# Performance work log

Hardware: AMD Instinct MI355X
Metric: run time of the kernel (lower is better)

Reference implementation:

```python
import jax, jax.numpy as jnp
import numpy as np

DIM, HEADS, SEQ_LEN = 768, 12, 4096
HEAD_DIM = DIM // HEADS
RMS_EPS = 1.1920928955078125e-07  # torch fp32 finfo eps (default for F.rms_norm)
ATTN_SCALE = 0.12


def _rms_norm(x):
    # F.rms_norm(x, (x.size(-1),)) with no weight
    return x * jax.lax.rsqrt(jnp.mean(x * x, axis=-1, keepdims=True) + RMS_EPS)


def _rotary_tables(T, head_dim):
    # angular_freq: (1/1024)**linspace(0,1,head_dim//4) padded with zeros to head_dim//2
    freqs = (1.0 / 1024.0) ** jnp.linspace(0.0, 1.0, head_dim // 4, dtype=jnp.float32)
    freqs = jnp.concatenate([freqs, jnp.zeros(head_dim // 4, dtype=jnp.float32)])
    t = jnp.arange(T, dtype=jnp.float32)
    theta = t[:, None] * freqs[None, :]  # [T, head_dim//2]
    return jnp.cos(theta), jnp.sin(theta)


def _apply_rotary(x, cos, sin):
    # x: [B, T, H, D]; cos/sin: [T, D//2]
    x1, x2 = jnp.split(x.astype(jnp.float32), 2, axis=-1)
    c = cos[None, :, None, :]
    s = sin[None, :, None, :]
    y1 = x1 * c + x2 * s
    y2 = -x1 * s + x2 * c
    return jnp.concatenate([y1, y2], axis=-1).astype(x.dtype)


def setup_inputs() -> dict:
    key = jax.random.key(0)
    k1, k2, k3 = jax.random.split(key, 3)
    x = jax.random.normal(k1, (1, SEQ_LEN, DIM), dtype=jnp.float32)
    std = 0.5 * DIM ** (-0.5)
    bound = (3.0 ** 0.5) * std
    qkv_w = jax.random.uniform(k2, (3, DIM, DIM), dtype=jnp.float32, minval=-bound, maxval=bound)
    # c_proj is zero-initialized in the module; use small random weights for a nontrivial baseline
    c_proj_w = jax.random.normal(k3, (DIM, DIM), dtype=jnp.float32) * (DIM ** -0.5)
    return {"x": x, "qkv_w": qkv_w, "c_proj_w": c_proj_w}


def reference(x, qkv_w, c_proj_w):
    B, T, dim = x.shape
    H, D = HEADS, HEAD_DIM
    # fused QKV: F.linear(x, qkv_w.flatten(end_dim=1)) -> x @ W^T, split into q,k,v
    qkv = jnp.einsum('btd,kfd->btkf', x, qkv_w)  # [B, T, 3, dim]
    qkv = qkv.reshape(B, T, 3, H, D)
    q, k, v = qkv[:, :, 0], qkv[:, :, 1], qkv[:, :, 2]  # each [B, T, H, D]
    q, k = _rms_norm(q), _rms_norm(k)
    cos, sin = _rotary_tables(T, D)
    q, k = _apply_rotary(q, cos, sin), _apply_rotary(k, cos, sin)
    # causal attention with scale=0.12 (flex_attention with causal block mask)
    scores = jnp.einsum('bthd,bshd->bhts', q, k) * ATTN_SCALE  # [B, H, T, T]
    causal = jnp.tril(jnp.ones((T, T), dtype=bool))
    scores = jnp.where(causal[None, None], scores, jnp.finfo(scores.dtype).min)
    probs = jax.nn.softmax(scores, axis=-1)
    y = jnp.einsum('bhts,bshd->bthd', probs, v).reshape(B, T, dim)
    return y @ c_proj_w.T
```

## Files before the change

kernel.cpp:

```cpp
#include <hip/hip_runtime.h>
#include <math.h>


typedef __bf16 bf16;
typedef __bf16 bf16x4 __attribute__((ext_vector_type(4)));
typedef __bf16 bf16x8 __attribute__((ext_vector_type(8)));
typedef float  f32x4  __attribute__((ext_vector_type(4)));

#define MFMA_BF16(a, b, c) __builtin_amdgcn_mfma_f32_16x16x32_bf16((a), (b), (c), 0, 0, 0)

#define SEQ  4096
#define NH   12
#define HD   64
#define DM   768
#define NQKV 2304
#define NPART 4
#define ATTN_SCALE 0.12f
#define LOG2E 1.4426950408889634f
#define RMS_EPS 1.1920928955078125e-07f

typedef __attribute__((address_space(3))) void  lds_void;
typedef const __attribute__((address_space(1))) void g_void;

__device__ __forceinline__ void gload16(const void* g, void* l)
{
  __builtin_amdgcn_global_load_lds((g_void*)g, (lds_void*)l, 16, 0, 0);
}

__global__ __launch_bounds__(256) void convert_in(const float* __restrict__ src,
                                                  bf16* __restrict__ dst, int n)
{
  const int i0 = (blockIdx.x * 256 + threadIdx.x) * 8;
  if (i0 >= n) return;
  f32x4 a = *(const f32x4*)(src + i0);
  f32x4 b = *(const f32x4*)(src + i0 + 4);
  bf16x8 o;
#pragma unroll
  for (int j = 0; j < 4; j++) { o[j] = (bf16)a[j]; o[j + 4] = (bf16)b[j]; }
  *(bf16x8*)(dst + i0) = o;
}

__device__ __forceinline__ void gemm128_core(
    const bf16* __restrict__ A, const bf16* __restrict__ B,
    int m0, int n0, bf16 (*As)[32], bf16 (*Bs)[32], f32x4 acc[4][4])
{
  const int tid = threadIdx.x;
  const int lane = tid & 63, w = tid >> 6;
  const int c16 = lane & 15, q4 = lane >> 4;
  const int mo = (w & 1) * 64, no = (w >> 1) * 64;
  const int srow = tid >> 2, scol = (tid & 3) * 8;
  const f32x4 vzero = {0.f, 0.f, 0.f, 0.f};
#pragma unroll
  for (int i = 0; i < 4; i++)
#pragma unroll
    for (int j = 0; j < 4; j++) acc[i][j] = vzero;

  const bf16* aBase = A + (size_t)(m0 + srow) * DM + scol;
  const bf16* bBase = B + (size_t)(n0 + srow) * DM + scol;

  for (int k0 = 0; k0 < DM; k0 += 32) {
    gload16(aBase + k0,                 &As[srow][scol]);
    gload16(aBase + (size_t)64 * DM + k0, &As[srow + 64][scol]);
    gload16(bBase + k0,                 &Bs[srow][scol]);
    gload16(bBase + (size_t)64 * DM + k0, &Bs[srow + 64][scol]);
    __syncthreads();
    bf16x8 ar[4], br[4];
#pragma unroll
    for (int mq = 0; mq < 4; mq++)
      ar[mq] = *(const bf16x8*)&As[mo + mq * 16 + c16][q4 * 8];
#pragma unroll
    for (int nq = 0; nq < 4; nq++)
      br[nq] = *(const bf16x8*)&Bs[no + nq * 16 + c16][q4 * 8];
#pragma unroll
    for (int mq = 0; mq < 4; mq++)
#pragma unroll
      for (int nq = 0; nq < 4; nq++)
        acc[mq][nq] = MFMA_BF16(ar[mq], br[nq], acc[mq][nq]);
    __syncthreads();
  }
}

__global__ __launch_bounds__(256) void gemm_qkv(
    const bf16* __restrict__ A, const bf16* __restrict__ B,
    bf16* __restrict__ Qb, bf16* __restrict__ Kb, bf16* __restrict__ Vt)
{
  __shared__ bf16 As[128][32];
  __shared__ bf16 Bs[128][32];
  const int m0 = blockIdx.x * 128, n0 = blockIdx.y * 128;
  f32x4 acc[4][4];
  gemm128_core(A, B, m0, n0, As, Bs, acc);

  const int lane = threadIdx.x & 63, w = threadIdx.x >> 6;
  const int c16 = lane & 15, q4 = lane >> 4;
  const int mo = (w & 1) * 64, no = (w >> 1) * 64;
  const int kidx = blockIdx.y / 6;
  const int rr0 = (n0 - kidx * DM) + no;
  const int h = rr0 >> 6;

  if (kidx == 2) {
#pragma unroll
    for (int nq = 0; nq < 4; nq++) {
      const int d = nq * 16 + c16;
#pragma unroll
      for (int mq = 0; mq < 4; mq++) {
        const int mb = m0 + mo + mq * 16 + q4 * 4;
#pragma unroll
        for (int rg = 0; rg < 4; rg++)
          Vt[((h * HD) + d) * SEQ + mb + rg] = (bf16)acc[mq][nq][rg];
      }
    }
  } else {
    bf16* dst = kidx ? Kb : Qb;
    const float scale = kidx ? 1.0f : (ATTN_SCALE * LOG2E);
    const float fr = exp2f(-10.0f * (float)c16 * (1.0f / 15.0f));
#pragma unroll
    for (int mq = 0; mq < 4; mq++) {
#pragma unroll
      for (int rg = 0; rg < 4; rg++) {
        const int m = m0 + mo + mq * 16 + q4 * 4 + rg;
        const float x0 = acc[mq][0][rg], x1 = acc[mq][1][rg];
        const float x2 = acc[mq][2][rg], x3 = acc[mq][3][rg];
        float ss = x0 * x0 + x1 * x1 + x2 * x2 + x3 * x3;
        ss += __shfl_xor(ss, 1, 64);
        ss += __shfl_xor(ss, 2, 64);
        ss += __shfl_xor(ss, 4, 64);
        ss += __shfl_xor(ss, 8, 64);
        const float rinv = rsqrtf(ss * (1.0f / 64.0f) + RMS_EPS) * scale;
        const float xn0 = x0 * rinv, xn1 = x1 * rinv;
        const float xn2 = x2 * rinv, xn3 = x3 * rinv;
        float sn, cs;
        sincosf((float)m * fr, &sn, &cs);
        const float y0 = xn0 * cs + xn2 * sn;
        const float y2 = xn2 * cs - xn0 * sn;
        bf16* rp = dst + (size_t)(h * SEQ + m) * HD + c16;
        rp[0]  = (bf16)y0;
        rp[16] = (bf16)xn1;
        rp[32] = (bf16)y2;
        rp[48] = (bf16)xn3;
      }
    }
  }
}

__global__ __launch_bounds__(256) void gemm_proj(
    const bf16* __restrict__ A, const bf16* __restrict__ B, float* __restrict__ C)
{
  __shared__ bf16 As[128][32];
  __shared__ bf16 Bs[128][32];
  const int m0 = blockIdx.x * 128, n0 = blockIdx.y * 128;
  f32x4 acc[4][4];
  gemm128_core(A, B, m0, n0, As, Bs, acc);

  const int lane = threadIdx.x & 63, w = threadIdx.x >> 6;
  const int c16 = lane & 15, q4 = lane >> 4;
  const int mo = (w & 1) * 64, no = (w >> 1) * 64;
#pragma unroll
  for (int nq = 0; nq < 4; nq++) {
    const int n = n0 + no + nq * 16 + c16;
#pragma unroll
    for (int mq = 0; mq < 4; mq++) {
      const int mb = m0 + mo + mq * 16 + q4 * 4;
#pragma unroll
      for (int rg = 0; rg < 4; rg++)
        C[(size_t)(mb + rg) * DM + n] = acc[mq][nq][rg];
    }
  }
}

__global__ __launch_bounds__(256, 3) void flash_partial(
    const bf16* __restrict__ Qb, const bf16* __restrict__ Kb,
    const bf16* __restrict__ Vt, bf16* __restrict__ Opart,
    float* __restrict__ Lpart)
{
  __shared__ bf16 Ks[64][72];
  __shared__ bf16 Vts[64][72];
  __shared__ bf16 Pst[4][32][68];
  const int h = blockIdx.y, p = blockIdx.z;
  const int jb = blockIdx.x;
  const int tid = threadIdx.x;
  const int lane = tid & 63, w = tid >> 6;
  const int c16 = lane & 15, q4 = lane >> 4;
  const int sr = tid >> 3, sc8 = (tid & 7) * 8;

  const bf16* Kbase = Kb + (size_t)h * SEQ * HD;
  const bf16* Vbase = Vt + (size_t)h * HD * SEQ;
  const f32x4 vzero = {0.f, 0.f, 0.f, 0.f};

#pragma unroll 1
  for (int half = 0; half < 2; ++half) {
    const int qi = half ? jb : (31 - jb);
    const int q0 = qi * 128;

    bf16x8 aq[2][2];
#pragma unroll
    for (int f = 0; f < 2; f++) {
      const int tq = q0 + w * 32 + f * 16 + c16;
      aq[f][0] = *(const bf16x8*)&Qb[((h * SEQ) + tq) * HD + q4 * 8];
      aq[f][1] = *(const bf16x8*)&Qb[((h * SEQ) + tq) * HD + 32 + q4 * 8];
    }
    const int qg[2] = { q0 + w * 32 + c16, q0 + w * 32 + 16 + c16 };
    const int qb[2] = { q0 + w * 32,       q0 + w * 32 + 16 };

    f32x4 O[2][4];
    float l_f[2] = {0.f, 0.f};
#pragma unroll
    for (int f = 0; f < 2; f++)
#pragma unroll
      for (int j = 0; j < 4; j++) O[f][j] = vzero;

    const int sEnd = q0 + 64;
    const int sBeg = p * 64;
    if (sBeg <= sEnd) {
      bf16x8 kr0 = *(const bf16x8*)&Kbase[(sBeg + sr) * HD + sc8];
      bf16x8 kr1 = *(const bf16x8*)&Kbase[(sBeg + sr + 32) * HD + sc8];
      bf16x8 vr0 = *(const bf16x8*)&Vbase[sr * SEQ + sBeg + sc8];
      bf16x8 vr1 = *(const bf16x8*)&Vbase[(sr + 32) * SEQ + sBeg + sc8];

      for (int s0 = sBeg; s0 <= sEnd; s0 += NPART * 64) {
        __syncthreads();
        *(bf16x8*)&Ks[sr][sc8]       = kr0;
        *(bf16x8*)&Ks[sr + 32][sc8]  = kr1;
        *(bf16x8*)&Vts[sr][sc8]      = vr0;
        *(bf16x8*)&Vts[sr + 32][sc8] = vr1;
        __syncthreads();

        const int snext = s0 + NPART * 64;
        if (snext <= sEnd) {
          kr0 = *(const bf16x8*)&Kbase[(snext + sr) * HD + sc8];
          kr1 = *(const bf16x8*)&Kbase[(snext + sr + 32) * HD + sc8];
          vr0 = *(const bf16x8*)&Vbase[sr * SEQ + snext + sc8];
          vr1 = *(const bf16x8*)&Vbase[(sr + 32) * SEQ + snext + sc8];
        }

        bf16x8 kf0[4], kf1[4];
#pragma unroll
        for (int nt = 0; nt < 4; nt++) {
          kf0[nt] = *(const bf16x8*)&Ks[nt * 16 + c16][q4 * 8];
          kf1[nt] = *(const bf16x8*)&Ks[nt * 16 + c16][32 + q4 * 8];
        }
#pragma unroll
        for (int f = 0; f < 2; f++) {
          f32x4 S[4];
          __builtin_amdgcn_s_setprio(1);
#pragma unroll
          for (int nt = 0; nt < 4; nt++) {
            f32x4 z = vzero;
            z = MFMA_BF16(kf0[nt], aq[f][0], z);
            z = MFMA_BF16(kf1[nt], aq[f][1], z);
            S[nt] = z;
          }
          __builtin_amdgcn_s_setprio(0);
          float lf = l_f[f];
          if (s0 + 63 <= qb[f]) {
#pragma unroll
            for (int nt = 0; nt < 4; nt++) {
#pragma unroll
              for (int rg = 0; rg < 4; rg++) {
                const float pv = exp2f(S[nt][rg]);
                S[nt][rg] = pv;
                lf += pv;
              }
              bf16x4 pk = { (bf16)S[nt][0], (bf16)S[nt][1], (bf16)S[nt][2], (bf16)S[nt][3] };
              *(bf16x4*)&Pst[w][f * 16 + c16][nt * 16 + q4 * 4] = pk;
            }
          } else if (s0 > qb[f] + 15) {
            const bf16x4 zk = { (bf16)0.f, (bf16)0.f, (bf16)0.f, (bf16)0.f };
#pragma unroll
            for (int nt = 0; nt < 4; nt++)
              *(bf16x4*)&Pst[w][f * 16 + c16][nt * 16 + q4 * 4] = zk;
          } else {
#pragma unroll
            for (int nt = 0; nt < 4; nt++) {
#pragma unroll
              for (int rg = 0; rg < 4; rg++) {
                const int s_g = s0 + nt * 16 + q4 * 4 + rg;
                const float pv = (s_g > qg[f]) ? 0.f : exp2f(S[nt][rg]);
                S[nt][rg] = pv;
                lf += pv;
              }
              bf16x4 pk = { (bf16)S[nt][0], (bf16)S[nt][1], (bf16)S[nt][2], (bf16)S[nt][3] };
              *(bf16x4*)&Pst[w][f * 16 + c16][nt * 16 + q4 * 4] = pk;
            }
          }
          l_f[f] = lf;
        }
        bf16x8 ap[2][2];
#pragma unroll
        for (int f = 0; f < 2; f++) {
          ap[f][0] = *(const bf16x8*)&Pst[w][f * 16 + c16][q4 * 8];
          ap[f][1] = *(const bf16x8*)&Pst[w][f * 16 + c16][32 + q4 * 8];
        }
#pragma unroll
        for (int dt = 0; dt < 4; dt++) {
          bf16x8 bv0 = *(const bf16x8*)&Vts[dt * 16 + c16][q4 * 8];
          bf16x8 bv1 = *(const bf16x8*)&Vts[dt * 16 + c16][32 + q4 * 8];
          __builtin_amdgcn_s_setprio(1);
#pragma unroll
          for (int f = 0; f < 2; f++) {
            O[f][dt] = MFMA_BF16(ap[f][0], bv0, O[f][dt]);
            O[f][dt] = MFMA_BF16(ap[f][1], bv1, O[f][dt]);
          }
          __builtin_amdgcn_s_setprio(0);
        }
      }
    }

#pragma unroll
    for (int f = 0; f < 2; f++) {
      float l = l_f[f];
      l += __shfl_xor(l, 16, 64);
      l += __shfl_xor(l, 32, 64);
      l_f[f] = l;
    }
    const int u = ((h * 32 + qi) * NPART + p);
    bf16* Op = Opart + (size_t)u * 8192;
#pragma unroll
    for (int f = 0; f < 2; f++)
#pragma unroll
      for (int dt = 0; dt < 4; dt++)
#pragma unroll
        for (int rg = 0; rg < 4; rg++)
          Op[(w * 32 + f * 16 + q4 * 4 + rg) * 64 + dt * 16 + c16] = (bf16)O[f][dt][rg];
    if (lane < 32) {
      if (q4 == 0) {
#pragma unroll
        for (int f = 0; f < 2; f++)
          Lpart[u * 128 + w * 32 + f * 16 + c16] = l_f[f];
      }
    }
  }
}

__global__ __launch_bounds__(256) void flash_combine(
    const bf16* __restrict__ Opart, const float* __restrict__ Lpart,
    bf16* __restrict__ Y)
{
  const int q64 = blockIdx.x, h = blockIdx.y;
  const int qi = q64 >> 1, roff = (q64 & 1) * 64;
  const int row = threadIdx.x >> 2, cg = (threadIdx.x & 3) * 16;
  const int u0 = (h * 32 + qi) * NPART;
  const int r128 = roff + row;
  float lsum = 0.f;
#pragma unroll
  for (int p = 0; p < NPART; p++) lsum += Lpart[(u0 + p) * 128 + r128];
  const float inv = 1.0f / lsum;
  const bf16* O0 = Opart + (size_t)u0 * 8192 + r128 * 64 + cg;
  bf16* yp = Y + (size_t)(q64 * 64 + row) * DM + h * HD + cg;
#pragma unroll
  for (int j = 0; j < 16; j += 8) {
    float s[8] = {0, 0, 0, 0, 0, 0, 0, 0};
#pragma unroll
    for (int p = 0; p < NPART; p++) {
      bf16x8 a = *(const bf16x8*)(O0 + p * 8192 + j);
#pragma unroll
      for (int e = 0; e < 8; e++) s[e] += (float)a[e];
    }
#pragma unroll
    for (int e = 0; e < 8; e++) yp[j + e] = (bf16)(s[e] * inv);
  }
}

extern "C" void kernel_launch(void* const* d_in, const int* in_sizes, int n_in,
                              void* d_out, int out_size, void* d_ws, size_t ws_size,
                              hipStream_t stream)
{
  (void)in_sizes; (void)n_in; (void)out_size; (void)ws_size;
  const float* x      = (const float*)d_in[0];
  const float* qkvw   = (const float*)d_in[1];
  const float* cprojw = (const float*)d_in[2];
  float* outp = (float*)d_out;

  const int NX = SEQ * DM, NW = NQKV * DM, NP = DM * DM;

  char* ws = (char*)d_ws;
  bf16*  xb    = (bf16*)(ws);
  bf16*  wqkv  = (bf16*)(ws + 6291456);
  bf16*  wproj = (bf16*)(ws + 9830400);
  bf16*  Q     = (bf16*)(ws + 11010048);
  bf16*  K     = (bf16*)(ws + 17301504);
  bf16*  Vt    = (bf16*)(ws + 23592960);
  bf16*  Y     = (bf16*)(ws + 29884416);
  bf16*  Opart = (bf16*)(ws + 36175872);
  float* Lpart = (float*)(ws + 61341696);

  convert_in<<<dim3(NX / 2048), 256, 0, stream>>>(x,      xb,    NX);
  convert_in<<<dim3(NW / 2048), 256, 0, stream>>>(qkvw,   wqkv,  NW);
  convert_in<<<dim3(NP / 2048), 256, 0, stream>>>(cprojw, wproj, NP);

  gemm_qkv     <<<dim3(SEQ / 128, NQKV / 128), 256, 0, stream>>>(xb, wqkv, Q, K, Vt);
  flash_partial<<<dim3(16, NH, NPART),         256, 0, stream>>>(Q, K, Vt, Opart, Lpart);
  flash_combine<<<dim3(SEQ / 64, NH),          256, 0, stream>>>(Opart, Lpart, Y);
  gemm_proj    <<<dim3(SEQ / 128, DM / 128),   256, 0, stream>>>(Y, wproj, outp);
}
```

Measured before the change: 180.5 us.

## Fuse input conversions, swizzle block order, retile projection GEMM, raise attention split count

The three fp32-to-bf16 conversion launches become one kernel that dispatches on block index. The QKV GEMM and flash attention kernels move to 1D grids with an XCD-style block swizzle, meant to improve L2 locality across chiplets. The projection GEMM drops to 64x64 tiles so more blocks fill the GPU. Attention now splits the key range into 5 parts instead of 4, and its occupancy hint rises from 3 to 4 blocks per CU. This adds combine work and partial buffer traffic and may cause register spilling under the tighter launch bound.

Result: slower. 208.2 us (+15.3%).

```diff
diff --git a/kernel.cpp b/kernel.cpp
--- a/kernel.cpp
+++ b/kernel.cpp
@@ -14,7 +14,7 @@
 #define HD   64
 #define DM   768
 #define NQKV 2304
-#define NPART 4
+#define NPART 5
 #define ATTN_SCALE 0.12f
 #define LOG2E 1.4426950408889634f
 #define RMS_EPS 1.1920928955078125e-07f
@@ -27,17 +27,24 @@
   __builtin_amdgcn_global_load_lds((g_void*)g, (lds_void*)l, 16, 0, 0);
 }
 
-__global__ __launch_bounds__(256) void convert_in(const float* __restrict__ src,
-                                                  bf16* __restrict__ dst, int n)
-{
-  const int i0 = (blockIdx.x * 256 + threadIdx.x) * 8;
-  if (i0 >= n) return;
-  f32x4 a = *(const f32x4*)(src + i0);
-  f32x4 b = *(const f32x4*)(src + i0 + 4);
+__global__ __launch_bounds__(256) void convert_all(
+    const float* __restrict__ s0, bf16* __restrict__ d0, int n0,
+    const float* __restrict__ s1, bf16* __restrict__ d1, int n1,
+    const float* __restrict__ s2, bf16* __restrict__ d2, int n2)
+{
+  int b = blockIdx.x;
+  const int b0 = n0 >> 11, b1 = n1 >> 11;
+  const float* s; bf16* d;
+  if (b < b0)            { s = s0; d = d0; }
+  else if (b < b0 + b1)  { s = s1; d = d1; b -= b0; }
+  else                   { s = s2; d = d2; b -= b0 + b1; }
+  const int i0 = (b * 256 + threadIdx.x) * 8;
+  f32x4 a = *(const f32x4*)(s + i0);
+  f32x4 c = *(const f32x4*)(s + i0 + 4);
   bf16x8 o;
 #pragma unroll
-  for (int j = 0; j < 4; j++) { o[j] = (bf16)a[j]; o[j + 4] = (bf16)b[j]; }
-  *(bf16x8*)(dst + i0) = o;
+  for (int j = 0; j < 4; j++) { o[j] = (bf16)a[j]; o[j + 4] = (bf16)c[j]; }
+  *(bf16x8*)(d + i0) = o;
 }
 
 __device__ __forceinline__ void gemm128_core(
@@ -59,9 +66,9 @@
   const bf16* bBase = B + (size_t)(n0 + srow) * DM + scol;
 
   for (int k0 = 0; k0 < DM; k0 += 32) {
-    gload16(aBase + k0,                 &As[srow][scol]);
+    gload16(aBase + k0,                   &As[srow][scol]);
     gload16(aBase + (size_t)64 * DM + k0, &As[srow + 64][scol]);
-    gload16(bBase + k0,                 &Bs[srow][scol]);
+    gload16(bBase + k0,                   &Bs[srow][scol]);
     gload16(bBase + (size_t)64 * DM + k0, &Bs[srow + 64][scol]);
     __syncthreads();
     bf16x8 ar[4], br[4];
@@ -86,14 +93,17 @@
 {
   __shared__ bf16 As[128][32];
   __shared__ bf16 Bs[128][32];
-  const int m0 = blockIdx.x * 128, n0 = blockIdx.y * 128;
+  const int id = blockIdx.x;
+  const int swz = (id & 7) * 72 + (id >> 3);
+  const int bx = swz & 31, by = swz >> 5;
+  const int m0 = bx * 128, n0 = by * 128;
   f32x4 acc[4][4];
   gemm128_core(A, B, m0, n0, As, Bs, acc);
 
   const int lane = threadIdx.x & 63, w = threadIdx.x >> 6;
   const int c16 = lane & 15, q4 = lane >> 4;
   const int mo = (w & 1) * 64, no = (w >> 1) * 64;
-  const int kidx = blockIdx.y / 6;
+  const int kidx = by / 6;
   const int rr0 = (n0 - kidx * DM) + no;
   const int h = rr0 >> 6;
 
@@ -145,20 +155,48 @@
 __global__ __launch_bounds__(256) void gemm_proj(
     const bf16* __restrict__ A, const bf16* __restrict__ B, float* __restrict__ C)
 {
-  __shared__ bf16 As[128][32];
-  __shared__ bf16 Bs[128][32];
-  const int m0 = blockIdx.x * 128, n0 = blockIdx.y * 128;
-  f32x4 acc[4][4];
-  gemm128_core(A, B, m0, n0, As, Bs, acc);
-
-  const int lane = threadIdx.x & 63, w = threadIdx.x >> 6;
+  __shared__ bf16 As[64][32];
+  __shared__ bf16 Bs[64][32];
+  const int m0 = blockIdx.x * 64, n0 = blockIdx.y * 64;
+  const int tid = threadIdx.x;
+  const int lane = tid & 63, w = tid >> 6;
   const int c16 = lane & 15, q4 = lane >> 4;
-  const int mo = (w & 1) * 64, no = (w >> 1) * 64;
-#pragma unroll
-  for (int nq = 0; nq < 4; nq++) {
+  const int mo = (w & 1) * 32, no = (w >> 1) * 32;
+  const int srow = tid >> 2, scol = (tid & 3) * 8;
+  const f32x4 vzero = {0.f, 0.f, 0.f, 0.f};
+  f32x4 acc[2][2];
+#pragma unroll
+  for (int i = 0; i < 2; i++)
+#pragma unroll
+    for (int j = 0; j < 2; j++) acc[i][j] = vzero;
+
+  const bf16* aBase = A + (size_t)(m0 + srow) * DM + scol;
+  const bf16* bBase = B + (size_t)(n0 + srow) * DM + scol;
+
+  for (int k0 = 0; k0 < DM; k0 += 32) {
+    gload16(aBase + k0, &As[srow][scol]);
+    gload16(bBase + k0, &Bs[srow][scol]);
+    __syncthreads();
+    bf16x8 ar[2], br[2];
+#pragma unroll
+    for (int mq = 0; mq < 2; mq++)
+      ar[mq] = *(const bf16x8*)&As[mo + mq * 16 + c16][q4 * 8];
+#pragma unroll
+    for (int nq = 0; nq < 2; nq++)
+      br[nq] = *(const bf16x8*)&Bs[no + nq * 16 + c16][q4 * 8];
+#pragma unroll
+    for (int mq = 0; mq < 2; mq++)
+#pragma unroll
+      for (int nq = 0; nq < 2; nq++)
+        acc[mq][nq] = MFMA_BF16(ar[mq], br[nq], acc[mq][nq]);
+    __syncthreads();
+  }
+
+#pragma unroll
+  for (int nq = 0; nq < 2; nq++) {
     const int n = n0 + no + nq * 16 + c16;
 #pragma unroll
-    for (int mq = 0; mq < 4; mq++) {
+    for (int mq = 0; mq < 2; mq++) {
       const int mb = m0 + mo + mq * 16 + q4 * 4;
 #pragma unroll
       for (int rg = 0; rg < 4; rg++)
@@ -167,7 +205,7 @@
   }
 }
 
-__global__ __launch_bounds__(256, 3) void flash_partial(
+__global__ __launch_bounds__(256, 4) void flash_partial(
     const bf16* __restrict__ Qb, const bf16* __restrict__ Kb,
     const bf16* __restrict__ Vt, bf16* __restrict__ Opart,
     float* __restrict__ Lpart)
@@ -175,8 +213,12 @@
   __shared__ bf16 Ks[64][72];
   __shared__ bf16 Vts[64][72];
   __shared__ bf16 Pst[4][32][68];
-  const int h = blockIdx.y, p = blockIdx.z;
-  const int jb = blockIdx.x;
+  const int id = blockIdx.x;
+  const int swz = (id & 7) * 120 + (id >> 3);
+  const int h = swz / 80;
+  const int rrem = swz - h * 80;
+  const int p = rrem >> 4;
+  const int jb = rrem & 15;
   const int tid = threadIdx.x;
   const int lane = tid & 63, w = tid >> 6;
   const int c16 = lane & 15, q4 = lane >> 4;
@@ -381,14 +423,13 @@
   bf16*  Vt    = (bf16*)(ws + 23592960);
   bf16*  Y     = (bf16*)(ws + 29884416);
   bf16*  Opart = (bf16*)(ws + 36175872);
-  float* Lpart = (float*)(ws + 61341696);
-
-  convert_in<<<dim3(NX / 2048), 256, 0, stream>>>(x,      xb,    NX);
-  convert_in<<<dim3(NW / 2048), 256, 0, stream>>>(qkvw,   wqkv,  NW);
-  convert_in<<<dim3(NP / 2048), 256, 0, stream>>>(cprojw, wproj, NP);
-
-  gemm_qkv     <<<dim3(SEQ / 128, NQKV / 128), 256, 0, stream>>>(xb, wqkv, Q, K, Vt);
-  flash_partial<<<dim3(16, NH, NPART),         256, 0, stream>>>(Q, K, Vt, Opart, Lpart);
-  flash_combine<<<dim3(SEQ / 64, NH),          256, 0, stream>>>(Opart, Lpart, Y);
-  gemm_proj    <<<dim3(SEQ / 128, DM / 128),   256, 0, stream>>>(Y, wproj, outp);
-}
+  float* Lpart = (float*)(ws + 67633152);
+
+  convert_all<<<dim3((NX + NW + NP) / 2048), 256, 0, stream>>>(
+      x, xb, NX, qkvw, wqkv, NW, cprojw, wproj, NP);
+
+  gemm_qkv     <<<dim3(32 * (NQKV / 128)),      256, 0, stream>>>(xb, wqkv, Q, K, Vt);
+  flash_partial<<<dim3(16 * NH * NPART),        256, 0, stream>>>(Q, K, Vt, Opart, Lpart);
+  flash_combine<<<dim3(SEQ / 64, NH),           256, 0, stream>>>(Opart, Lpart, Y);
+  gemm_proj    <<<dim3(SEQ / 64, DM / 64),      256, 0, stream>>>(Y, wproj, outp);
+}
```
